# Kernel optimization log

Measured on AMD Instinct MI355X. Metric: run time of the kernel, lower is better.

## Reference

```python
import jax, jax.numpy as jnp
import numpy as np

D = 256  # feature_dim
B, N = 16, 1024
NEG_SLOPE = 0.2
SCALE = float(np.sqrt(D))


def setup_inputs() -> dict:
    key = jax.random.key(0)
    ks = jax.random.split(key, 8)
    s = 1.0 / np.sqrt(D)  # torch Linear default init scale
    return {
        "feature": jax.random.normal(ks[0], (B, N, D), dtype=jnp.float32),
        "graph": jax.random.randint(ks[1], (B, N, N), 0, 2, dtype=jnp.int32),
        "W_w": jax.random.uniform(ks[2], (D, D), jnp.float32, -s, s),
        "W_b": jax.random.uniform(ks[3], (D,), jnp.float32, -s, s),
        "Q_w": jax.random.uniform(ks[4], (D, D), jnp.float32, -s, s),
        "Q_b": jax.random.uniform(ks[5], (D,), jnp.float32, -s, s),
        "K_w": jax.random.uniform(ks[6], (D, D), jnp.float32, -s, s),
        "K_b": jax.random.uniform(ks[7], (D,), jnp.float32, -s, s),
    }


def reference(feature, graph, W_w, W_b, Q_w, Q_b, K_w, K_b):
    # h = W(feature); torch Linear: x @ W.T + b
    h = jnp.einsum('bnd,ed->bne', feature, W_w) + W_b        # [B,N,D]
    q = jnp.einsum('bnd,ed->bne', h, Q_w) + Q_b              # [B,N,D]
    k = jnp.einsum('bnd,ed->bne', h, K_w) + K_b              # [B,N,D]
    e = jnp.einsum('bnd,bmd->bnm', q, k) / SCALE             # [B,N,N]
    e = jnp.where(e >= 0, e, NEG_SLOPE * e)                  # LeakyReLU(0.2)
    e = jnp.where(graph == 0, jnp.float32(-1e9), e)          # mask
    a = jax.nn.softmax(e, axis=2)                            # dropout = identity (eval)
    out = jax.nn.relu(jnp.einsum('bnm,bmd->bnd', a, h))      # [B,N,D]
    return out
```

## Files before the change

### kernel.cpp

```cpp
#include <hip/hip_runtime.h>
#include <hip/hip_bf16.h>
#include <stdint.h>

#define DD 256
#define NB 16
#define NN 1024
#define MTOT (NB * NN)

typedef __attribute__((ext_vector_type(8))) short short8;
typedef __attribute__((ext_vector_type(4))) float f32x4;

__device__ __forceinline__ ushort f2b(float f) {
  uint32_t u = __float_as_uint(f);
  return (ushort)((u + 0x7fffu + ((u >> 16) & 1u)) >> 16);
}

__device__ __forceinline__ void stage_weights(const float* __restrict__ W,
                                              ushort* Wl, int tid) {
  for (int i = 0; i < 64; ++i) {
    int idx4 = i * 256 + tid;
    int row = idx4 >> 6;
    int col0 = (idx4 & 63) << 2;
    float4 v = ((const float4*)W)[idx4];
    ushort4 b4;
    b4.x = f2b(v.x); b4.y = f2b(v.y); b4.z = f2b(v.z); b4.w = f2b(v.w);
    int byte = (row * 512 + col0 * 2) ^ ((row & 7) << 4);
    *(ushort4*)((char*)Wl + byte) = b4;
  }
}

__global__ __launch_bounds__(256, 1) void gemm_fused(
    const float* __restrict__ feature, const float* __restrict__ W_w,
    const float* __restrict__ W_b, const float* __restrict__ Q_w,
    const float* __restrict__ Q_b, const float* __restrict__ K_w,
    const float* __restrict__ K_b, ushort* __restrict__ hT,
    ushort* __restrict__ q, ushort* __restrict__ k) {
  __shared__ ushort Wl[256 * 256];
  const int tid = threadIdx.x;
  const int w = tid >> 6, lane = tid & 63, l15 = lane & 15, hi = lane >> 4;
  const int m0 = blockIdx.x * 64 + w * 16;
  const int arow = m0 + l15;

  stage_weights(W_w, Wl, tid);
  __syncthreads();

  f32x4 acc[16] = {};
#pragma unroll
  for (int kk = 0; kk < 8; ++kk) {
    const int k0 = kk * 32 + hi * 8;
    const float4* ap = (const float4*)(feature + arow * 256 + k0);
    float4 x = ap[0], y = ap[1];
    short8 a;
    a[0] = (short)f2b(x.x); a[1] = (short)f2b(x.y);
    a[2] = (short)f2b(x.z); a[3] = (short)f2b(x.w);
    a[4] = (short)f2b(y.x); a[5] = (short)f2b(y.y);
    a[6] = (short)f2b(y.z); a[7] = (short)f2b(y.w);
#pragma unroll
    for (int et = 0; et < 16; ++et) {
      int er = et * 16 + l15;
      short8 bf = *(const short8*)((const char*)Wl +
                                   ((er * 512 + k0 * 2) ^ ((er & 7) << 4)));
      acc[et] = __builtin_amdgcn_mfma_f32_16x16x32_bf16(a, bf, acc[et], 0, 0, 0);
    }
  }

  ushort hvals[16][4];
#pragma unroll
  for (int et = 0; et < 16; ++et) {
    float bv = W_b[et * 16 + l15];
#pragma unroll
    for (int r = 0; r < 4; ++r) hvals[et][r] = f2b(acc[et][r] + bv);
  }

  __syncthreads();
  ushort* Tl = Wl;
  {
    const int mloc = w * 16 + hi * 4;
#pragma unroll
    for (int et = 0; et < 16; ++et)
#pragma unroll
      for (int r = 0; r < 4; ++r)
        Tl[(et * 16 + l15) * 64 + mloc + r] = hvals[et][r];
  }
  __syncthreads();

  short8 qa[8];
#pragma unroll
  for (int kk = 0; kk < 8; ++kk) {
    const int k0 = kk * 32 + hi * 8;
#pragma unroll
    for (int j = 0; j < 8; ++j)
      qa[kk][j] = (short)Tl[(k0 + j) * 64 + w * 16 + l15];
  }
  {
    const int bidx = blockIdx.x >> 4;
    const int n0 = (blockIdx.x & 15) * 64;
    ushort* dst = hT + bidx * (256 * 1024) + tid * 1024 + n0;
    const uint4* src = (const uint4*)(Tl + tid * 64);
#pragma unroll
    for (int j = 0; j < 8; ++j) ((uint4*)dst)[j] = src[j];
  }
  __syncthreads();

  stage_weights(Q_w, Wl, tid);
  __syncthreads();
#pragma unroll
  for (int et = 0; et < 16; ++et) acc[et] = (f32x4){0.f, 0.f, 0.f, 0.f};
#pragma unroll
  for (int kk = 0; kk < 8; ++kk) {
    const int k0 = kk * 32 + hi * 8;
#pragma unroll
    for (int et = 0; et < 16; ++et) {
      int er = et * 16 + l15;
      short8 bf = *(const short8*)((const char*)Wl +
                                   ((er * 512 + k0 * 2) ^ ((er & 7) << 4)));
      acc[et] = __builtin_amdgcn_mfma_f32_16x16x32_bf16(qa[kk], bf, acc[et], 0, 0, 0);
    }
  }
#pragma unroll
  for (int et = 0; et < 16; ++et) {
    int e = et * 16 + l15;
    float bv = Q_b[e];
#pragma unroll
    for (int r = 0; r < 4; ++r)
      q[(m0 + hi * 4 + r) * 256 + e] = f2b(acc[et][r] + bv);
  }
  __syncthreads();

  stage_weights(K_w, Wl, tid);
  __syncthreads();
#pragma unroll
  for (int et = 0; et < 16; ++et) acc[et] = (f32x4){0.f, 0.f, 0.f, 0.f};
#pragma unroll
  for (int kk = 0; kk < 8; ++kk) {
    const int k0 = kk * 32 + hi * 8;
#pragma unroll
    for (int et = 0; et < 16; ++et) {
      int er = et * 16 + l15;
      short8 bf = *(const short8*)((const char*)Wl +
                                   ((er * 512 + k0 * 2) ^ ((er & 7) << 4)));
      acc[et] = __builtin_amdgcn_mfma_f32_16x16x32_bf16(qa[kk], bf, acc[et], 0, 0, 0);
    }
  }
#pragma unroll
  for (int et = 0; et < 16; ++et) {
    int e = et * 16 + l15;
    float bv = K_b[e];
#pragma unroll
    for (int r = 0; r < 4; ++r)
      k[(m0 + hi * 4 + r) * 256 + e] = f2b(acc[et][r] + bv);
  }
}

#define SM_KT 0
#define SM_HT 32768
#define SM_PL 65536
#define SM_M2 73728
#define SM_CM 74752
#define SM_SZ 75008

__device__ __forceinline__ int pswz(int row, int bytecol) {
  return (row * 64 + bytecol) ^ ((row & 7) << 4) ^ ((row >> 3) << 5);
}

__global__ __launch_bounds__(512, 2) void attn8(
    const ushort* __restrict__ Q, const ushort* __restrict__ Kb,
    const ushort* __restrict__ HT, const int* __restrict__ graph,
    float* __restrict__ out) {
  __shared__ __align__(16) char smem[SM_SZ];
  ushort* Kt = (ushort*)(smem + SM_KT);
  ushort* Ht = (ushort*)(smem + SM_HT);
  ushort* Pl = (ushort*)(smem + SM_PL);
  uint* M2 = (uint*)(smem + SM_M2);
  float* Cm = (float*)(smem + SM_CM);

  const int tid = threadIdx.x;
  const int w = tid >> 6, lane = tid & 63, l15 = lane & 15, hi = lane >> 4;
  const int wg = w >> 1, half = w & 1;
  const int hw = blockIdx.x;
  const int slot = hw >> 3;
  const int b = (hw & 7) * 2 + (slot >> 4);
  const int q0 = (slot & 15) * 64;
  const int qrow_a = q0 + wg * 16 + l15;
  const int qrow_cl = wg * 16 + hi * 4;
  const int* grow_base = graph + (b * 1024 + q0 + w * 8) * 1024 + lane;

  int greg[8];

#pragma unroll
  for (int j = 0; j < 8; ++j) greg[j] = grow_base[j * 1024];

  short8 qf[8];
#pragma unroll
  for (int kk = 0; kk < 8; ++kk)
    qf[kk] = *(const short8*)(Q + (b * 1024 + qrow_a) * 256 + kk * 32 + hi * 8);

#pragma unroll
  for (int j = 0; j < 8; ++j) {
    unsigned long long mm = __ballot(greg[j] != 0);
    if (lane == 0) {
      M2[(w * 8 + j) * 2] = (uint)mm;
      M2[(w * 8 + j) * 2 + 1] = (uint)(mm >> 32);
    }
  }

  float lR[4] = {0.f, 0.f, 0.f, 0.f};
  f32x4 o[16] = {};

  for (int t = 0; t < 16; ++t) {
    const uint* M2c = M2 + (t & 1) * 128;
    uint* M2n = M2 + ((t & 1) ^ 1) * 128;

    __syncthreads();
#pragma unroll
    for (int i = 0; i < 4; ++i) {
      int c = i * 512 + tid;
      int krow = c >> 5, col0 = (c & 31) << 3;
      uint4 v = *(const uint4*)(Kb + (b * 1024 + t * 64 + krow) * 256 + col0);
      *(uint4*)((char*)Kt + ((krow * 512 + col0 * 2) ^ ((krow & 7) << 4))) = v;
    }
#pragma unroll
    for (int i = 0; i < 4; ++i) {
      int c = i * 512 + tid;
      int drow = c >> 3, col0 = (c & 7) << 3;
      uint4 v = *(const uint4*)(HT + b * (256 * 1024) + drow * 1024 + t * 64 + col0);
      *(uint4*)((char*)Ht + ((drow * 128 + col0 * 2) ^ ((drow & 7) << 4))) = v;
    }
    __syncthreads();

    if (t < 15) {
#pragma unroll
      for (int j = 0; j < 8; ++j) greg[j] = grow_base[j * 1024 + (t + 1) * 64];
    }

    f32x4 s[2] = {};
    __builtin_amdgcn_s_setprio(1);
#pragma unroll
    for (int kk = 0; kk < 8; ++kk) {
#pragma unroll
      for (int nt = 0; nt < 2; ++nt) {
        int krow = half * 32 + nt * 16 + l15;
        short8 kf = *(const short8*)((const char*)Kt +
            ((krow * 512 + (kk * 32 + hi * 8) * 2) ^ ((krow & 7) << 4)));
        s[nt] = __builtin_amdgcn_mfma_f32_16x16x32_bf16(qf[kk], kf, s[nt], 0, 0, 0);
      }
    }
    __builtin_amdgcn_s_setprio(0);

    float p[2][4];
#pragma unroll
    for (int r = 0; r < 4; ++r) {
      uint mw = M2c[(qrow_cl + r) * 2 + half];
      float v0 = s[0][r] * 0.0625f; v0 = (v0 >= 0.f) ? v0 : 0.2f * v0;
      float v1 = s[1][r] * 0.0625f; v1 = (v1 >= 0.f) ? v1 : 0.2f * v1;
      float p0 = ((mw >> l15) & 1u) ? __expf(v0) : 0.f;
      float p1 = ((mw >> (16 + l15)) & 1u) ? __expf(v1) : 0.f;
      p[0][r] = p0; p[1][r] = p1;
      lR[r] += p0 + p1;
    }

    ushort* Pw = Pl + w * 512;
#pragma unroll
    for (int nt = 0; nt < 2; ++nt)
#pragma unroll
      for (int r = 0; r < 4; ++r) {
        int row = hi * 4 + r, col = nt * 16 + l15;
        *(ushort*)((char*)Pw + pswz(row, col * 2)) = f2b(p[nt][r]);
      }
    __asm__ volatile("s_waitcnt lgkmcnt(0)" ::: "memory");
    short8 pa = *(const short8*)((const char*)Pw + pswz(l15, hi * 16));

    __builtin_amdgcn_s_setprio(1);
#pragma unroll
    for (int dt = 0; dt < 16; ++dt) {
      int dcol = dt * 16 + l15;
      short8 hf = *(const short8*)((const char*)Ht +
          ((dcol * 128 + (half * 32 + hi * 8) * 2) ^ ((dcol & 7) << 4)));
      o[dt] = __builtin_amdgcn_mfma_f32_16x16x32_bf16(pa, hf, o[dt], 0, 0, 0);
    }
    __builtin_amdgcn_s_setprio(0);

    if (t < 15) {
#pragma unroll
      for (int j = 0; j < 8; ++j) {
        unsigned long long mm = __ballot(greg[j] != 0);
        if (lane == 0) {
          M2n[(w * 8 + j) * 2] = (uint)mm;
          M2n[(w * 8 + j) * 2 + 1] = (uint)(mm >> 32);
        }
      }
    }
  }

#pragma unroll
  for (int r = 0; r < 4; ++r) {
    lR[r] += __shfl_xor(lR[r], 1);
    lR[r] += __shfl_xor(lR[r], 2);
    lR[r] += __shfl_xor(lR[r], 4);
    lR[r] += __shfl_xor(lR[r], 8);
  }

  __syncthreads();
  float* Ob = (float*)smem;
  if (half == 1) {
#pragma unroll
    for (int dt = 0; dt < 16; ++dt)
#pragma unroll
      for (int r = 0; r < 4; ++r) {
        int row = hi * 4 + r;
        int byte = (row * 1024 + (dt * 16 + l15) * 4) ^ ((row & 15) << 6);
        *(float*)((char*)Ob + wg * 16384 + byte) = o[dt][r];
      }
    if (l15 == 0) {
#pragma unroll
      for (int r = 0; r < 4; ++r)
        Cm[wg * 16 + hi * 4 + r] = lR[r];
    }
  }
  __syncthreads();
  if (half == 0) {
#pragma unroll
    for (int r = 0; r < 4; ++r) {
      int rowl = hi * 4 + r;
      float inv = 1.f / (lR[r] + Cm[wg * 16 + rowl]);
      int orow = b * 1024 + q0 + wg * 16 + rowl;
#pragma unroll
      for (int dt = 0; dt < 16; ++dt) {
        int byte = (rowl * 1024 + (dt * 16 + l15) * 4) ^ ((rowl & 15) << 6);
        float ob = *(const float*)((const char*)Ob + wg * 16384 + byte);
        float v = (o[dt][r] + ob) * inv;
        out[orow * 256 + dt * 16 + l15] = fmaxf(v, 0.f);
      }
    }
  }
}

extern "C" void kernel_launch(void* const* d_in, const int* in_sizes, int n_in,
                              void* d_out, int out_size, void* d_ws,
                              size_t ws_size, hipStream_t stream) {
  const float* feature = (const float*)d_in[0];
  const int* graph = (const int*)d_in[1];
  const float* W_w = (const float*)d_in[2];
  const float* W_b = (const float*)d_in[3];
  const float* Q_w = (const float*)d_in[4];
  const float* Q_b = (const float*)d_in[5];
  const float* K_w = (const float*)d_in[6];
  const float* K_b = (const float*)d_in[7];
  float* out = (float*)d_out;

  ushort* hT = (ushort*)d_ws;
  ushort* q = hT + MTOT * DD;
  ushort* k = q + MTOT * DD;

  gemm_fused<<<256, 256, 0, stream>>>(feature, W_w, W_b, Q_w, Q_b, K_w, K_b,
                                      hT, q, k);
  attn8<<<256, 512, 0, stream>>>(q, k, hT, graph, out);
}
```

Before: 93.69 us.

## Double-buffer K and H tiles in LDS to overlap staging with compute

Splits the K and H^T tiles in shared memory into two buffers and stages the next tile at the end of each iteration, so each loop step needs one barrier instead of two. The goal is to overlap global loads for tile t+1 with the tail of tile t's MFMA work and to cut barrier stalls. Shared memory grows from about 75KB to about 140KB per block, which prevents two 512-thread blocks from sharing a CU as the launch bounds request and so lowers occupancy. The staging loads are still issued synchronously after the compute of each iteration rather than prefetched into registers early, so little latency may actually be hidden.

Result: faster. 91.14 us (-2.7%).

```diff
diff --git a/kernel.cpp b/kernel.cpp
--- a/kernel.cpp
+++ b/kernel.cpp
@@ -152,12 +152,14 @@
   }
 }
 
-#define SM_KT 0
-#define SM_HT 32768
-#define SM_PL 65536
-#define SM_M2 73728
-#define SM_CM 74752
-#define SM_SZ 75008
+#define SM_KT0 0
+#define SM_KT1 32768
+#define SM_HT0 65536
+#define SM_HT1 98304
+#define SM_PL 131072
+#define SM_M2 139264
+#define SM_CM 140288
+#define SM_SZ 140544
 
 __device__ __forceinline__ int pswz(int row, int bytecol) {
   return (row * 64 + bytecol) ^ ((row & 7) << 4) ^ ((row >> 3) << 5);
@@ -168,8 +170,6 @@
     const ushort* __restrict__ HT, const int* __restrict__ graph,
     float* __restrict__ out) {
   __shared__ __align__(16) char smem[SM_SZ];
-  ushort* Kt = (ushort*)(smem + SM_KT);
-  ushort* Ht = (ushort*)(smem + SM_HT);
   ushort* Pl = (ushort*)(smem + SM_PL);
   uint* M2 = (uint*)(smem + SM_M2);
   float* Cm = (float*)(smem + SM_CM);
@@ -187,8 +187,32 @@
 
   int greg[8];
 
+#define STAGE_TILE(tt, bb)                                                    \
+  {                                                                           \
+    ushort* Kd = (ushort*)(smem + ((bb) ? SM_KT1 : SM_KT0));                  \
+    ushort* Hd = (ushort*)(smem + ((bb) ? SM_HT1 : SM_HT0));                  \
+    _Pragma("unroll") for (int i = 0; i < 4; ++i) {                           \
+      int c = i * 512 + tid;                                                  \
+      int krow = c >> 5, col0 = (c & 31) << 3;                                \
+      uint4 v =                                                               \
+          *(const uint4*)(Kb + (b * 1024 + (tt) * 64 + krow) * 256 + col0);   \
+      *(uint4*)((char*)Kd + ((krow * 512 + col0 * 2) ^ ((krow & 7) << 4))) =  \
+          v;                                                                  \
+    }                                                                         \
+    _Pragma("unroll") for (int i = 0; i < 4; ++i) {                           \
+      int c = i * 512 + tid;                                                  \
+      int drow = c >> 3, col0 = (c & 7) << 3;                                 \
+      uint4 v = *(const uint4*)(HT + b * (256 * 1024) + drow * 1024 +         \
+                                (tt) * 64 + col0);                            \
+      *(uint4*)((char*)Hd + ((drow * 128 + col0 * 2) ^ ((drow & 7) << 4))) =  \
+          v;                                                                  \
+    }                                                                         \
+  }
+
 #pragma unroll
   for (int j = 0; j < 8; ++j) greg[j] = grow_base[j * 1024];
+
+  STAGE_TILE(0, 0);
 
   short8 qf[8];
 #pragma unroll
@@ -207,26 +231,14 @@
   float lR[4] = {0.f, 0.f, 0.f, 0.f};
   f32x4 o[16] = {};
 
+  __syncthreads();
+
   for (int t = 0; t < 16; ++t) {
-    const uint* M2c = M2 + (t & 1) * 128;
-    uint* M2n = M2 + ((t & 1) ^ 1) * 128;
-
-    __syncthreads();
-#pragma unroll
-    for (int i = 0; i < 4; ++i) {
-      int c = i * 512 + tid;
-      int krow = c >> 5, col0 = (c & 31) << 3;
-      uint4 v = *(const uint4*)(Kb + (b * 1024 + t * 64 + krow) * 256 + col0);
-      *(uint4*)((char*)Kt + ((krow * 512 + col0 * 2) ^ ((krow & 7) << 4))) = v;
-    }
-#pragma unroll
-    for (int i = 0; i < 4; ++i) {
-      int c = i * 512 + tid;
-      int drow = c >> 3, col0 = (c & 7) << 3;
-      uint4 v = *(const uint4*)(HT + b * (256 * 1024) + drow * 1024 + t * 64 + col0);
-      *(uint4*)((char*)Ht + ((drow * 128 + col0 * 2) ^ ((drow & 7) << 4))) = v;
-    }
-    __syncthreads();
+    const int cur = t & 1;
+    const ushort* Kt = (const ushort*)(smem + (cur ? SM_KT1 : SM_KT0));
+    const ushort* Ht = (const ushort*)(smem + (cur ? SM_HT1 : SM_HT0));
+    const uint* M2c = M2 + cur * 128;
+    uint* M2n = M2 + (cur ^ 1) * 128;
 
     if (t < 15) {
 #pragma unroll
@@ -289,7 +301,10 @@
           M2n[(w * 8 + j) * 2 + 1] = (uint)(mm >> 32);
         }
       }
-    }
+      STAGE_TILE(t + 1, cur ^ 1);
+    }
+
+    __syncthreads();
   }
 
 #pragma unroll
@@ -300,7 +315,6 @@
     lR[r] += __shfl_xor(lR[r], 8);
   }
 
-  __syncthreads();
   float* Ob = (float*)smem;
   if (half == 1) {
 #pragma unroll
@@ -333,6 +347,7 @@
       }
     }
   }
+#undef STAGE_TILE
 }
 
 extern "C" void kernel_launch(void* const* d_in, const int* in_sizes, int n_in,
```
